# Kernel tuning notes

Hardware: AMD Instinct MI355X
Metric: run time of the kernel (lower is better)

Reference implementation:

```python
import jax, jax.numpy as jnp
import numpy as np

B, N, DIM, H, DH, PD = 2, 1024, 768, 8, 64, 4
EPS = 1e-8


def setup_inputs() -> dict:
    key = jax.random.key(0)
    ks = jax.random.split(key, 12)
    w = lambda k, shp: jax.random.normal(k, shp, dtype=jnp.float32) * 0.02
    return {
        "x": jax.random.normal(ks[0], (B, N, DIM), dtype=jnp.float32),
        "rotations": jax.random.normal(ks[1], (B, N, 3, 3), dtype=jnp.float32),
        "translations": jax.random.normal(ks[2], (B, N, 3), dtype=jnp.float32),
        "W_sq": w(ks[3], (H * DH, DIM)),
        "W_sk": w(ks[4], (H * DH, DIM)),
        "W_sv": w(ks[5], (H * DH, DIM)),
        "W_pq": w(ks[6], (H * PD * 3, DIM)),
        "W_pk": w(ks[7], (H * PD * 3, DIM)),
        "W_pv": w(ks[8], (H * PD * 3, DIM)),
        "point_weights": jax.random.normal(ks[9], (H,), dtype=jnp.float32),
        "W_out": w(ks[10], (DIM, H * (DH + PD * 4))),
        "b_out": jax.random.normal(ks[11], (DIM,), dtype=jnp.float32) * 0.02,
    }


def reference(x, rotations, translations, W_sq, W_sk, W_sv, W_pq, W_pk, W_pv, point_weights, W_out, b_out):
    b, n, _ = x.shape
    h, dh, pd = H, DH, PD
    scalar_scale = (2 * dh) ** -0.5           # num_attn_logits=2
    point_scale = (2 * pd * (9 / 2)) ** -0.5

    # scalar q/k/v: [b,h,n,dh]
    qs = (x @ W_sq.T).reshape(b, n, h, dh).transpose(0, 2, 1, 3)
    ks = (x @ W_sk.T).reshape(b, n, h, dh).transpose(0, 2, 1, 3)
    vs = (x @ W_sv.T).reshape(b, n, h, dh).transpose(0, 2, 1, 3)

    # point q/k/v: [b,h,n,pd,3]
    qp = (x @ W_pq.T).reshape(b, n, h, pd, 3).transpose(0, 2, 1, 3, 4)
    kp = (x @ W_pk.T).reshape(b, n, h, pd, 3).transpose(0, 2, 1, 3, 4)
    vp = (x @ W_pv.T).reshape(b, n, h, pd, 3).transpose(0, 2, 1, 3, 4)

    t = translations[:, None, :, None, :]  # [b,1,n,1,3]
    # global-frame points: p_c = sum_r R[n,c,r] * p[d,r] + t
    qp = jnp.einsum('bncr,bhndr->bhndc', rotations, qp) + t
    kp = jnp.einsum('bncr,bhndr->bhndc', rotations, kp) + t
    vp = jnp.einsum('bncr,bhndr->bhndc', rotations, vp) + t

    # scalar attention logits [b,h,i,j]
    logits = jnp.einsum('bhid,bhjd->bhij', qs, ks) * scalar_scale

    # point distance term: sum_{d,c} (q-k)^2 = |q|^2 + |k|^2 - 2 q.k (no [i,j,d,c] tensor)
    q2 = jnp.sum(qp ** 2, axis=(-1, -2))  # [b,h,i]
    k2 = jnp.sum(kp ** 2, axis=(-1, -2))  # [b,h,j]
    qk = jnp.einsum('bhidc,bhjdc->bhij', qp, kp)
    point_dist = q2[..., :, None] + k2[..., None, :] - 2.0 * qk

    pw = jax.nn.softplus(point_weights)[None, :, None, None]  # [1,h,1,1]
    logits = logits - 0.5 * (point_dist * pw * point_scale)

    attn = jax.nn.softmax(logits, axis=-1)

    rs = jnp.einsum('bhij,bhjd->bhid', attn, vs)          # [b,h,n,dh]
    rp = jnp.einsum('bhij,bhjdc->bhidc', attn, vp)        # [b,h,n,pd,3]
    # back to local frame: R^T (p - t)
    rp = jnp.einsum('bnrc,bhndr->bhndc', rotations, rp - t)
    rn = jnp.sqrt(jnp.sum(rp ** 2, axis=-1) + EPS)        # [b,h,n,pd]

    rs = rs.transpose(0, 2, 1, 3).reshape(b, n, h * dh)
    rp_f = rp.transpose(0, 2, 1, 3, 4).reshape(b, n, h * pd * 3)
    rn = rn.transpose(0, 2, 1, 3).reshape(b, n, h * pd)

    results = jnp.concatenate([rs, rp_f, rn], axis=-1)    # [b,n,640]
    return results @ W_out.T + b_out
```

## Files before the change

### kernel.cpp

```cpp
#include <hip/hip_runtime.h>
#include <hip/hip_bf16.h>
#include <math.h>

#define B_  2
#define N_  1024
#define DIM_ 768
#define H_  8
#define DH_ 64
#define PD_ 4
#define NPROJ 1824
#define NPAD  1920
#define BH_ (B_*H_)
#define FDIM 640

#define OFF_RS   0u
#define OFF_RP   (OFF_RS + (size_t)BH_*N_*DH_)
#define OFF_PRAW (OFF_RP + (size_t)BH_*N_*12)
#define OFF_QA   (OFF_PRAW + (size_t)B_*N_*288)
#define OFF_KA   (OFF_QA + (size_t)BH_*N_*96/2)
#define OFF_VT   (OFF_KA + (size_t)BH_*N_*96/2)
#define OFF_XB   (OFF_VT + (size_t)BH_*80*N_/2)
#define OFF_WB   (OFF_XB + (size_t)B_*N_*DIM_/2)
#define OFF_FB   OFF_XB
#define OFF_WOB  OFF_WB

typedef __attribute__((ext_vector_type(8))) short bf16x8;
typedef __attribute__((ext_vector_type(4))) float f32x4;

__device__ __forceinline__ float dot4(float4 a, float4 b) {
    return a.x*b.x + a.y*b.y + a.z*b.z + a.w*b.w;
}
__device__ __forceinline__ unsigned short f2bf(float f) {
    __hip_bfloat16 h = __float2bfloat16(f);
    return *reinterpret_cast<unsigned short*>(&h);
}

__global__ __launch_bounds__(256) void k_cvt_x(
    const float* __restrict__ x, unsigned short* __restrict__ xb)
{
    int i = blockIdx.x * 256 + threadIdx.x;
    if (i >= (B_*N_*DIM_)/4) return;
    float4 v = reinterpret_cast<const float4*>(x)[i];
    ushort4 o;
    o.x = f2bf(v.x); o.y = f2bf(v.y); o.z = f2bf(v.z); o.w = f2bf(v.w);
    reinterpret_cast<ushort4*>(xb)[i] = o;
}

__global__ __launch_bounds__(256) void k_cvt_w(
    const float* __restrict__ Wsq, const float* __restrict__ Wsk,
    const float* __restrict__ Wsv, const float* __restrict__ Wpq,
    const float* __restrict__ Wpk, const float* __restrict__ Wpv,
    unsigned short* __restrict__ wb)
{
    int i = blockIdx.x * 256 + threadIdx.x;
    if (i >= (NPAD*DIM_)/4) return;
    int row = i / (DIM_/4);
    int c4  = i % (DIM_/4);
    ushort4 o;
    if (row >= NPROJ) {
        o.x = o.y = o.z = o.w = 0;
    } else {
        const float* W;
        if      (row < 512)  W = Wsq + (size_t)row*DIM_;
        else if (row < 1024) W = Wsk + (size_t)(row-512)*DIM_;
        else if (row < 1536) W = Wsv + (size_t)(row-1024)*DIM_;
        else if (row < 1632) W = Wpq + (size_t)(row-1536)*DIM_;
        else if (row < 1728) W = Wpk + (size_t)(row-1632)*DIM_;
        else                 W = Wpv + (size_t)(row-1728)*DIM_;
        float4 v = reinterpret_cast<const float4*>(W)[c4];
        o.x = f2bf(v.x); o.y = f2bf(v.y); o.z = f2bf(v.z); o.w = f2bf(v.w);
    }
    reinterpret_cast<ushort4*>(wb)[i] = o;
}

__global__ __launch_bounds__(256) void k_cvt_wout(
    const float* __restrict__ Wout, unsigned short* __restrict__ wob)
{
    int i = blockIdx.x * 256 + threadIdx.x;
    if (i >= (DIM_*FDIM)/4) return;
    float4 v = reinterpret_cast<const float4*>(Wout)[i];
    ushort4 o;
    o.x = f2bf(v.x); o.y = f2bf(v.y); o.z = f2bf(v.z); o.w = f2bf(v.w);
    reinterpret_cast<ushort4*>(wob)[i] = o;
}

__global__ __launch_bounds__(256) void k_proj_mfma(
    const unsigned short* __restrict__ xb,
    const unsigned short* __restrict__ wb,
    float* __restrict__ ws)
{
    __shared__ unsigned short sAB[2*128*32];
    const int tid  = threadIdx.x;
    const int lane = tid & 63;
    const int wid  = tid >> 6;
    const int mt = blockIdx.x & 15;
    const int nt = blockIdx.x >> 4;
    const int row0 = mt*128;
    const int col0 = nt*128;
    const int wr = (wid >> 1)*64;
    const int wc = (wid & 1)*64;

    f32x4 acc[4][4];
    #pragma unroll
    for (int m = 0; m < 4; ++m)
        #pragma unroll
        for (int n = 0; n < 4; ++n) acc[m][n] = (f32x4){0.f,0.f,0.f,0.f};

    for (int kt = 0; kt < DIM_/32; ++kt) {
        __syncthreads();
        #pragma unroll
        for (int t = 0; t < 4; ++t) {
            int chunk = t*4 + wid;
            int tile  = chunk >> 3;
            int crow  = (chunk & 7) * 16;
            int grow  = (tile ? col0 : row0) + crow + (lane >> 2);
            const unsigned short* gsrc = (tile ? wb : xb)
                + (size_t)grow*DIM_ + kt*32 + (lane & 3)*8;
            __builtin_amdgcn_global_load_lds(
                (const __attribute__((address_space(1))) void*)gsrc,
                (__attribute__((address_space(3))) void*)(sAB + chunk*512),
                16, 0, 0);
        }
        __syncthreads();

        bf16x8 a[4], b[4];
        #pragma unroll
        for (int m = 0; m < 4; ++m)
            a[m] = *reinterpret_cast<const bf16x8*>(
                sAB + ((wr + m*16 + (lane & 15))*32 + (lane >> 4)*8));
        #pragma unroll
        for (int n = 0; n < 4; ++n)
            b[n] = *reinterpret_cast<const bf16x8*>(
                sAB + 128*32 + ((wc + n*16 + (lane & 15))*32 + (lane >> 4)*8));
        #pragma unroll
        for (int m = 0; m < 4; ++m)
            #pragma unroll
            for (int n = 0; n < 4; ++n)
                acc[m][n] = __builtin_amdgcn_mfma_f32_16x16x32_bf16(
                    a[m], b[n], acc[m][n], 0, 0, 0);
    }

    unsigned short* qa = (unsigned short*)(ws + OFF_QA);
    unsigned short* ka = (unsigned short*)(ws + OFF_KA);
    unsigned short* vt = (unsigned short*)(ws + OFF_VT);
    float* praw = ws + OFF_PRAW;
    const float ss = 0.08838834764831845f;

    #pragma unroll
    for (int n = 0; n < 4; ++n) {
        int o = col0 + wc + n*16 + (lane & 15);
        if (o >= NPROJ) continue;
        #pragma unroll
        for (int m = 0; m < 4; ++m) {
            #pragma unroll
            for (int j = 0; j < 4; ++j) {
                int r = row0 + wr + m*16 + (lane >> 4)*4 + j;
                int bb = r >> 10, nn = r & (N_-1);
                float v = acc[m][n][j];
                if (o < 512) {
                    int h = o >> 6, c = o & 63;
                    qa[((size_t)(bb*H_ + h)*N_ + nn)*96 + c] = f2bf(v*ss);
                } else if (o < 1024) {
                    int oo = o - 512; int h = oo >> 6, c = oo & 63;
                    ka[((size_t)(bb*H_ + h)*N_ + nn)*96 + c] = f2bf(v);
                } else if (o < 1536) {
                    int oo = o - 1024; int h = oo >> 6, c = oo & 63;
                    vt[((size_t)(bb*H_ + h)*80 + c)*N_ + nn] = f2bf(v);
                } else {
                    praw[(size_t)r*288 + (o - 1536)] = v;
                }
            }
        }
    }
}

__global__ __launch_bounds__(128) void k_prep(
    const float* __restrict__ rot_g,
    const float* __restrict__ trans_g,
    const float* __restrict__ pw_g,
    float* __restrict__ ws)
{
    __shared__ float R[9], T[3];
    __shared__ float rot[3][8][4][3];
    __shared__ float p2[2][8][4];
    __shared__ float q2t[8], k2t[8], coefs[8];
    const int tid = threadIdx.x;
    const int row = blockIdx.x;
    const int b = row >> 10, n = row & (N_-1);

    if (tid < 9)  R[tid] = rot_g[(size_t)row*9 + tid];
    if (tid >= 9 && tid < 12) T[tid-9] = trans_g[(size_t)row*3 + (tid-9)];
    if (tid >= 16 && tid < 24) {
        float pw = pw_g[tid-16];
        coefs[tid-16] = 0.5f * log1pf(__expf(pw)) * (1.0f/6.0f);
    }
    __syncthreads();
    if (tid < 96) {
        int which = tid >> 5, idx = tid & 31;
        int h = idx >> 2, pd = idx & 3;
        const float* p = ws + OFF_PRAW + (size_t)row*288 + which*96 + h*12 + pd*3;
        float px = p[0], py = p[1], pz = p[2];
        float c0 = R[0]*px + R[1]*py + R[2]*pz + T[0];
        float c1 = R[3]*px + R[4]*py + R[5]*pz + T[1];
        float c2 = R[6]*px + R[7]*py + R[8]*pz + T[2];
        rot[which][h][pd][0] = c0;
        rot[which][h][pd][1] = c1;
        rot[which][h][pd][2] = c2;
        if (which < 2) p2[which][h][pd] = c0*c0 + c1*c1 + c2*c2;
    }
    __syncthreads();
    if (tid < 16) {
        int w = tid >> 3, h = tid & 7;
        float s = p2[w][h][0] + p2[w][h][1] + p2[w][h][2] + p2[w][h][3];
        if (w) k2t[h] = s; else q2t[h] = s;
    }
    __syncthreads();

    unsigned short* qa = (unsigned short*)(ws + OFF_QA);
    unsigned short* ka = (unsigned short*)(ws + OFF_KA);
    unsigned short* vt = (unsigned short*)(ws + OFF_VT);

    for (int i = tid; i < 256; i += 128) {
        int h = i >> 5, c = i & 31;
        float qv, kv;
        if (c < 12)      { qv = rot[0][h][c/3][c%3] * 2.f * coefs[h]; kv = rot[1][h][c/3][c%3]; }
        else if (c == 12){ qv = q2t[h];  kv = -coefs[h]; }
        else if (c == 13){ qv = 1.f;     kv = -coefs[h]*k2t[h]; }
        else             { qv = 0.f;     kv = 0.f; }
        size_t base = ((size_t)(b*H_ + h)*N_ + n)*96 + 64 + c;
        qa[base] = f2bf(qv);
        ka[base] = f2bf(kv);
    }
    {
        int h = tid >> 4, r = tid & 15;
        float vv = (r < 12) ? rot[2][h][r/3][r%3] : 0.f;
        vt[((size_t)(b*H_ + h)*80 + 64 + r)*N_ + n] = f2bf(vv);
    }
}

#define VPAD 72
#define APAD 84
__global__ __launch_bounds__(512, 4) void k_attn_mfma(
    const unsigned short* __restrict__ qa_g,
    const unsigned short* __restrict__ ka_g,
    const unsigned short* __restrict__ vt_g,
    float* __restrict__ ws)
{
    __shared__ unsigned short sP[8][16*VPAD];
    __shared__ float sAcc[3][2][16][APAD];
    __shared__ float sML[3][2][16][2];

    const int tid  = threadIdx.x;
    const int lane = tid & 63;
    const int wid  = tid >> 6;
    const int lo = lane & 15;
    const int hi = lane >> 4;
    const int bid = blockIdx.x;
    const int Lb = (bid & 7)*64 + (bid >> 3);
    const int bh = Lb >> 5;
    const int qt = Lb & 31;
    const int q0 = qt * 32;
    const int qh = wid & 1;
    const int kq = wid >> 1;
    const int mrow = qh * 16;

    const unsigned short* Qa = qa_g + (size_t)bh*N_*96;
    const unsigned short* Ka = ka_g + (size_t)bh*N_*96;
    const unsigned short* Vt = vt_g + (size_t)bh*80*N_;

    bf16x8 qfr[3];
    {
        int qrow = q0 + mrow + lo;
        #pragma unroll
        for (int c = 0; c < 3; ++c)
            qfr[c] = *reinterpret_cast<const bf16x8*>(
                Qa + (size_t)qrow*96 + c*32 + hi*8);
    }

    f32x4 acc[5];
    #pragma unroll
    for (int d = 0; d < 5; ++d) acc[d] = (f32x4){0.f,0.f,0.f,0.f};
    float m[4] = {-1e30f,-1e30f,-1e30f,-1e30f};
    float l[4] = {0.f,0.f,0.f,0.f};

    for (int it = 0; it < 4; ++it) {
        const int j0 = (kq*4 + it)*64;

        bf16x8 kb[3][4];
        #pragma unroll
        for (int c = 0; c < 3; ++c)
            #pragma unroll
            for (int t = 0; t < 4; ++t)
                kb[c][t] = *reinterpret_cast<const bf16x8*>(
                    Ka + (size_t)(j0 + t*16 + lo)*96 + c*32 + hi*8);

        f32x4 s[4];
        #pragma unroll
        for (int t = 0; t < 4; ++t) s[t] = (f32x4){0.f,0.f,0.f,0.f};
        #pragma unroll
        for (int c = 0; c < 3; ++c)
            #pragma unroll
            for (int t = 0; t < 4; ++t)
                s[t] = __builtin_amdgcn_mfma_f32_16x16x32_bf16(qfr[c], kb[c][t], s[t], 0, 0, 0);

        bf16x8 vb[2][5];
        #pragma unroll
        for (int kk = 0; kk < 2; ++kk)
            #pragma unroll
            for (int dt = 0; dt < 5; ++dt)
                vb[kk][dt] = *reinterpret_cast<const bf16x8*>(
                    Vt + (size_t)(dt*16 + lo)*N_ + j0 + kk*32 + hi*8);

        float scl[4];
        #pragma unroll
        for (int r = 0; r < 4; ++r) {
            float v = fmaxf(fmaxf(s[0][r], s[1][r]), fmaxf(s[2][r], s[3][r]));
            v = fmaxf(v, __shfl_xor(v, 1));
            v = fmaxf(v, __shfl_xor(v, 2));
            v = fmaxf(v, __shfl_xor(v, 4));
            v = fmaxf(v, __shfl_xor(v, 8));
            float mn = fmaxf(m[r], v);
            scl[r] = __expf(m[r] - mn);
            m[r] = mn;
        }
        float ps[4] = {0.f,0.f,0.f,0.f};
        #pragma unroll
        for (int t = 0; t < 4; ++t) {
            #pragma unroll
            for (int r = 0; r < 4; ++r) {
                float p = __expf(s[t][r] - m[r]);
                ps[r] += p;
                sP[wid][(hi*4 + r)*VPAD + t*16 + lo] = f2bf(p);
            }
        }
        #pragma unroll
        for (int r = 0; r < 4; ++r) {
            float v = ps[r];
            v += __shfl_xor(v, 1);
            v += __shfl_xor(v, 2);
            v += __shfl_xor(v, 4);
            v += __shfl_xor(v, 8);
            l[r] = l[r]*scl[r] + v;
        }
        #pragma unroll
        for (int d = 0; d < 5; ++d)
            #pragma unroll
            for (int r = 0; r < 4; ++r) acc[d][r] *= scl[r];

        #pragma unroll
        for (int kk = 0; kk < 2; ++kk) {
            bf16x8 pa = *reinterpret_cast<const bf16x8*>(
                &sP[wid][lo*VPAD + kk*32 + hi*8]);
            #pragma unroll
            for (int dt = 0; dt < 5; ++dt)
                acc[dt] = __builtin_amdgcn_mfma_f32_16x16x32_bf16(pa, vb[kk][dt], acc[dt], 0, 0, 0);
        }
    }

    if (kq > 0) {
        #pragma unroll
        for (int r = 0; r < 4; ++r) {
            int rl = hi*4 + r;
            #pragma unroll
            for (int dt = 0; dt < 5; ++dt)
                sAcc[kq-1][qh][rl][dt*16 + lo] = acc[dt][r];
            if (lo == 0) { sML[kq-1][qh][rl][0] = m[r]; sML[kq-1][qh][rl][1] = l[r]; }
        }
    }
    __syncthreads();
    if (kq == 0) {
        float* ws_rs = ws + OFF_RS + (size_t)bh*N_*DH_;
        float* ws_rp = ws + OFF_RP + (size_t)bh*N_*12;
        #pragma unroll
        for (int r = 0; r < 4; ++r) {
            int rl = hi*4 + r;
            float mp[3], lp[3];
            float mm = m[r];
            #pragma unroll
            for (int p = 0; p < 3; ++p) {
                mp[p] = sML[p][qh][rl][0];
                lp[p] = sML[p][qh][rl][1];
                mm = fmaxf(mm, mp[p]);
            }
            float f0 = __expf(m[r] - mm);
            float Lsum = l[r]*f0;
            float fp[3];
            #pragma unroll
            for (int p = 0; p < 3; ++p) {
                fp[p] = __expf(mp[p] - mm);
                Lsum += lp[p]*fp[p];
            }
            float inv = 1.f / Lsum;
            int i = q0 + mrow + rl;
            #pragma unroll
            for (int dt = 0; dt < 5; ++dt) {
                float val = acc[dt][r]*f0;
                #pragma unroll
                for (int p = 0; p < 3; ++p)
                    val += sAcc[p][qh][rl][dt*16 + lo]*fp[p];
                val *= inv;
                int d = dt*16 + lo;
                if (d < 64)
                    ws_rs[(size_t)i*DH_ + d] = val;
                else if (d - 64 < 12)
                    ws_rp[(size_t)i*12 + (d - 64)] = val;
            }
        }
    }
}

__global__ __launch_bounds__(256) void k_fin_prep(
    const float* __restrict__ rotations,
    const float* __restrict__ translations,
    const float* __restrict__ ws,
    unsigned short* __restrict__ fb)
{
    __shared__ float sF[8][FDIM];
    const int tid = threadIdx.x;
    const int row0 = blockIdx.x * 8;
    const int b = row0 >> 10;
    const float* ws_rs = ws + OFF_RS;
    const float* ws_rp = ws + OFF_RP;

    for (int i = tid; i < 8*512; i += 256) {
        int r = i >> 9, f = i & 511;
        int h = f >> 6, c = f & 63;
        int n = (row0 & (N_-1)) + r;
        sF[r][f] = ws_rs[(((size_t)(b*H_ + h))*N_ + n)*DH_ + c];
    }
    {
        int r = tid >> 5;
        int idx = tid & 31;
        int h = idx >> 2, pd = idx & 3;
        int row = row0 + r;
        int n = row & (N_-1);
        const float* rp = ws_rp + (((size_t)(b*H_ + h))*N_ + n)*12 + pd*3;
        const float* R = rotations + (size_t)row*9;
        const float* T = translations + (size_t)row*3;
        float d0 = rp[0] - T[0], d1 = rp[1] - T[1], d2 = rp[2] - T[2];
        float l0 = R[0]*d0 + R[3]*d1 + R[6]*d2;
        float l1 = R[1]*d0 + R[4]*d1 + R[7]*d2;
        float l2 = R[2]*d0 + R[5]*d1 + R[8]*d2;
        sF[r][512 + h*12 + pd*3 + 0] = l0;
        sF[r][512 + h*12 + pd*3 + 1] = l1;
        sF[r][512 + h*12 + pd*3 + 2] = l2;
        sF[r][608 + h*4 + pd] = sqrtf(l0*l0 + l1*l1 + l2*l2 + 1e-8f);
    }
    __syncthreads();

    #pragma unroll
    for (int r = 0; r < 8; ++r) {
        for (int f = tid; f < FDIM; f += 256) {
            fb[(size_t)(row0 + r)*FDIM + f] = f2bf(sF[r][f]);
        }
    }
}

__global__ __launch_bounds__(256) void k_out_mfma(
    const unsigned short* __restrict__ fb,
    const unsigned short* __restrict__ wob,
    const float* __restrict__ bout,
    float* __restrict__ out)
{
    __shared__ unsigned short sAB[2*128*32];
    const int tid  = threadIdx.x;
    const int lane = tid & 63;
    const int wid  = tid >> 6;
    const int mt = blockIdx.x & 15;
    const int nt = blockIdx.x >> 4;
    const int row0 = mt*128;
    const int col0 = nt*128;
    const int wr = (wid >> 1)*64;
    const int wc = (wid & 1)*64;

    f32x4 acc[4][4];
    #pragma unroll
    for (int m = 0; m < 4; ++m)
        #pragma unroll
        for (int n = 0; n < 4; ++n) acc[m][n] = (f32x4){0.f,0.f,0.f,0.f};

    for (int kt = 0; kt < FDIM/32; ++kt) {
        __syncthreads();
        #pragma unroll
        for (int t = 0; t < 4; ++t) {
            int chunk = t*4 + wid;
            int tile  = chunk >> 3;
            int crow  = (chunk & 7) * 16;
            int grow  = (tile ? col0 : row0) + crow + (lane >> 2);
            const unsigned short* gsrc = (tile ? wob : fb)
                + (size_t)grow*FDIM + kt*32 + (lane & 3)*8;
            __builtin_amdgcn_global_load_lds(
                (const __attribute__((address_space(1))) void*)gsrc,
                (__attribute__((address_space(3))) void*)(sAB + chunk*512),
                16, 0, 0);
        }
        __syncthreads();

        bf16x8 a[4], b[4];
        #pragma unroll
        for (int m = 0; m < 4; ++m)
            a[m] = *reinterpret_cast<const bf16x8*>(
                sAB + ((wr + m*16 + (lane & 15))*32 + (lane >> 4)*8));
        #pragma unroll
        for (int n = 0; n < 4; ++n)
            b[n] = *reinterpret_cast<const bf16x8*>(
                sAB + 128*32 + ((wc + n*16 + (lane & 15))*32 + (lane >> 4)*8));
        #pragma unroll
        for (int m = 0; m < 4; ++m)
            #pragma unroll
            for (int n = 0; n < 4; ++n)
                acc[m][n] = __builtin_amdgcn_mfma_f32_16x16x32_bf16(
                    a[m], b[n], acc[m][n], 0, 0, 0);
    }

    #pragma unroll
    for (int n = 0; n < 4; ++n) {
        int o = col0 + wc + n*16 + (lane & 15);
        float bo = bout[o];
        #pragma unroll
        for (int m = 0; m < 4; ++m) {
            #pragma unroll
            for (int j = 0; j < 4; ++j) {
                int r = row0 + wr + m*16 + (lane >> 4)*4 + j;
                out[(size_t)r*DIM_ + o] = acc[m][n][j] + bo;
            }
        }
    }
}

extern "C" void kernel_launch(void* const* d_in, const int* in_sizes, int n_in,
                              void* d_out, int out_size, void* d_ws, size_t ws_size,
                              hipStream_t stream) {
    const float* x            = (const float*)d_in[0];
    const float* rotations    = (const float*)d_in[1];
    const float* translations = (const float*)d_in[2];
    const float* Wsq          = (const float*)d_in[3];
    const float* Wsk          = (const float*)d_in[4];
    const float* Wsv          = (const float*)d_in[5];
    const float* Wpq          = (const float*)d_in[6];
    const float* Wpk          = (const float*)d_in[7];
    const float* Wpv          = (const float*)d_in[8];
    const float* pweights     = (const float*)d_in[9];
    const float* Wout         = (const float*)d_in[10];
    const float* bout         = (const float*)d_in[11];
    float* out = (float*)d_out;
    float* ws  = (float*)d_ws;

    unsigned short* xb  = (unsigned short*)(ws + OFF_XB);
    unsigned short* wb  = (unsigned short*)(ws + OFF_WB);
    unsigned short* qa  = (unsigned short*)(ws + OFF_QA);
    unsigned short* ka  = (unsigned short*)(ws + OFF_KA);
    unsigned short* vt  = (unsigned short*)(ws + OFF_VT);
    unsigned short* fb  = (unsigned short*)(ws + OFF_FB);
    unsigned short* wob = (unsigned short*)(ws + OFF_WOB);

    k_cvt_x<<<(B_*N_*DIM_/4 + 255)/256, 256, 0, stream>>>(x, xb);
    k_cvt_w<<<(NPAD*DIM_/4 + 255)/256, 256, 0, stream>>>(Wsq, Wsk, Wsv, Wpq, Wpk, Wpv, wb);
    k_proj_mfma<<<16*15, 256, 0, stream>>>(xb, wb, ws);
    k_prep<<<B_*N_, 128, 0, stream>>>(rotations, translations, pweights, ws);
    k_attn_mfma<<<BH_*32, 512, 0, stream>>>(qa, ka, vt, ws);
    k_cvt_wout<<<(DIM_*FDIM/4 + 255)/256, 256, 0, stream>>>(Wout, wob);
    k_fin_prep<<<B_*N_/8, 256, 0, stream>>>(rotations, translations, ws, fb);
    k_out_mfma<<<16*6, 256, 0, stream>>>(fb, wob, bout, out);
}
```

Measured before the change: 100.9 us.

## Replace LDS-staged GEMMs with single-wave direct-register MFMA tiles and XCD-aware mapping

Both the projection GEMM and the output GEMM drop the shared-memory staged 128x128 tiles with four waves. Each block is now a single wave computing a 64x64 tile, loading fragments directly from global memory into registers with a two-stage double buffer. Block indices are remapped so consecutive tiles land on the same XCD. This removes LDS traffic and barriers and raises the block count to fill more CUs. The cost is no operand sharing between waves, so global and L2 traffic per FLOP goes up.

```diff
diff --git a/kernel.cpp b/kernel.cpp
--- a/kernel.cpp
+++ b/kernel.cpp
@@ -27,9 +27,6 @@
 typedef __attribute__((ext_vector_type(8))) short bf16x8;
 typedef __attribute__((ext_vector_type(4))) float f32x4;
 
-__device__ __forceinline__ float dot4(float4 a, float4 b) {
-    return a.x*b.x + a.y*b.y + a.z*b.z + a.w*b.w;
-}
 __device__ __forceinline__ unsigned short f2bf(float f) {
     __hip_bfloat16 h = __float2bfloat16(f);
     return *reinterpret_cast<unsigned short*>(&h);
@@ -84,21 +81,47 @@
     reinterpret_cast<ushort4*>(wob)[i] = o;
 }
 
-__global__ __launch_bounds__(256) void k_proj_mfma(
+__device__ __forceinline__ void load_frags(
+    const unsigned short* __restrict__ A0,
+    const unsigned short* __restrict__ B0,
+    int koff, int ld, bf16x8 a[4], bf16x8 b[4])
+{
+    #pragma unroll
+    for (int m = 0; m < 4; ++m)
+        a[m] = *reinterpret_cast<const bf16x8*>(A0 + (size_t)m*16*ld + koff);
+    #pragma unroll
+    for (int n = 0; n < 4; ++n)
+        b[n] = *reinterpret_cast<const bf16x8*>(B0 + (size_t)n*16*ld + koff);
+}
+
+__device__ __forceinline__ void mfma16(
+    const bf16x8 a[4], const bf16x8 b[4], f32x4 acc[4][4])
+{
+    #pragma unroll
+    for (int m = 0; m < 4; ++m)
+        #pragma unroll
+        for (int n = 0; n < 4; ++n)
+            acc[m][n] = __builtin_amdgcn_mfma_f32_16x16x32_bf16(
+                a[m], b[n], acc[m][n], 0, 0, 0);
+}
+
+__global__ __launch_bounds__(64, 1) void k_proj_mfma(
     const unsigned short* __restrict__ xb,
     const unsigned short* __restrict__ wb,
     float* __restrict__ ws)
 {
-    __shared__ unsigned short sAB[2*128*32];
-    const int tid  = threadIdx.x;
-    const int lane = tid & 63;
-    const int wid  = tid >> 6;
-    const int mt = blockIdx.x & 15;
-    const int nt = blockIdx.x >> 4;
-    const int row0 = mt*128;
-    const int col0 = nt*128;
-    const int wr = (wid >> 1)*64;
-    const int wc = (wid & 1)*64;
+    const int lane = threadIdx.x;
+    const int lo = lane & 15;
+    const int hi = lane >> 4;
+    const int bid = blockIdx.x;
+    const int L = (bid & 7)*120 + (bid >> 3);
+    const int mt = L / 30;
+    const int nt = L % 30;
+    const int row0 = mt*64;
+    const int col0 = nt*64;
+
+    const unsigned short* A0 = xb + (size_t)(row0 + lo)*DIM_ + hi*8;
+    const unsigned short* B0 = wb + (size_t)(col0 + lo)*DIM_ + hi*8;
 
     f32x4 acc[4][4];
     #pragma unroll
@@ -106,38 +129,14 @@
         #pragma unroll
         for (int n = 0; n < 4; ++n) acc[m][n] = (f32x4){0.f,0.f,0.f,0.f};
 
-    for (int kt = 0; kt < DIM_/32; ++kt) {
-        __syncthreads();
-        #pragma unroll
-        for (int t = 0; t < 4; ++t) {
-            int chunk = t*4 + wid;
-            int tile  = chunk >> 3;
-            int crow  = (chunk & 7) * 16;
-            int grow  = (tile ? col0 : row0) + crow + (lane >> 2);
-            const unsigned short* gsrc = (tile ? wb : xb)
-                + (size_t)grow*DIM_ + kt*32 + (lane & 3)*8;
-            __builtin_amdgcn_global_load_lds(
-                (const __attribute__((address_space(1))) void*)gsrc,
-                (__attribute__((address_space(3))) void*)(sAB + chunk*512),
-                16, 0, 0);
-        }
-        __syncthreads();
-
-        bf16x8 a[4], b[4];
-        #pragma unroll
-        for (int m = 0; m < 4; ++m)
-            a[m] = *reinterpret_cast<const bf16x8*>(
-                sAB + ((wr + m*16 + (lane & 15))*32 + (lane >> 4)*8));
-        #pragma unroll
-        for (int n = 0; n < 4; ++n)
-            b[n] = *reinterpret_cast<const bf16x8*>(
-                sAB + 128*32 + ((wc + n*16 + (lane & 15))*32 + (lane >> 4)*8));
-        #pragma unroll
-        for (int m = 0; m < 4; ++m)
-            #pragma unroll
-            for (int n = 0; n < 4; ++n)
-                acc[m][n] = __builtin_amdgcn_mfma_f32_16x16x32_bf16(
-                    a[m], b[n], acc[m][n], 0, 0, 0);
+    bf16x8 aA[4], bA[4], aB[4], bB[4];
+    load_frags(A0, B0, 0, DIM_, aA, bA);
+    for (int kt = 0; kt < DIM_/32; kt += 2) {
+        load_frags(A0, B0, (kt+1)*32, DIM_, aB, bB);
+        mfma16(aA, bA, acc);
+        if (kt + 2 < DIM_/32)
+            load_frags(A0, B0, (kt+2)*32, DIM_, aA, bA);
+        mfma16(aB, bB, acc);
     }
 
     unsigned short* qa = (unsigned short*)(ws + OFF_QA);
@@ -148,13 +147,13 @@
 
     #pragma unroll
     for (int n = 0; n < 4; ++n) {
-        int o = col0 + wc + n*16 + (lane & 15);
+        int o = col0 + n*16 + lo;
         if (o >= NPROJ) continue;
         #pragma unroll
         for (int m = 0; m < 4; ++m) {
             #pragma unroll
             for (int j = 0; j < 4; ++j) {
-                int r = row0 + wr + m*16 + (lane >> 4)*4 + j;
+                int r = row0 + m*16 + hi*4 + j;
                 int bb = r >> 10, nn = r & (N_-1);
                 float v = acc[m][n][j];
                 if (o < 512) {
@@ -456,22 +455,24 @@
     }
 }
 
-__global__ __launch_bounds__(256) void k_out_mfma(
+__global__ __launch_bounds__(64, 1) void k_out_mfma(
     const unsigned short* __restrict__ fb,
     const unsigned short* __restrict__ wob,
     const float* __restrict__ bout,
     float* __restrict__ out)
 {
-    __shared__ unsigned short sAB[2*128*32];
-    const int tid  = threadIdx.x;
-    const int lane = tid & 63;
-    const int wid  = tid >> 6;
-    const int mt = blockIdx.x & 15;
-    const int nt = blockIdx.x >> 4;
-    const int row0 = mt*128;
-    const int col0 = nt*128;
-    const int wr = (wid >> 1)*64;
-    const int wc = (wid & 1)*64;
+    const int lane = threadIdx.x;
+    const int lo = lane & 15;
+    const int hi = lane >> 4;
+    const int bid = blockIdx.x;
+    const int L = (bid & 7)*48 + (bid >> 3);
+    const int mt = L / 12;
+    const int nt = L % 12;
+    const int row0 = mt*64;
+    const int col0 = nt*64;
+
+    const unsigned short* A0 = fb  + (size_t)(row0 + lo)*FDIM + hi*8;
+    const unsigned short* B0 = wob + (size_t)(col0 + lo)*FDIM + hi*8;
 
     f32x4 acc[4][4];
     #pragma unroll
@@ -479,49 +480,25 @@
         #pragma unroll
         for (int n = 0; n < 4; ++n) acc[m][n] = (f32x4){0.f,0.f,0.f,0.f};
 
-    for (int kt = 0; kt < FDIM/32; ++kt) {
-        __syncthreads();
-        #pragma unroll
-        for (int t = 0; t < 4; ++t) {
-            int chunk = t*4 + wid;
-            int tile  = chunk >> 3;
-            int crow  = (chunk & 7) * 16;
-            int grow  = (tile ? col0 : row0) + crow + (lane >> 2);
-            const unsigned short* gsrc = (tile ? wob : fb)
-                + (size_t)grow*FDIM + kt*32 + (lane & 3)*8;
-            __builtin_amdgcn_global_load_lds(
-                (const __attribute__((address_space(1))) void*)gsrc,
-                (__attribute__((address_space(3))) void*)(sAB + chunk*512),
-                16, 0, 0);
-        }
-        __syncthreads();
-
-        bf16x8 a[4], b[4];
-        #pragma unroll
-        for (int m = 0; m < 4; ++m)
-            a[m] = *reinterpret_cast<const bf16x8*>(
-                sAB + ((wr + m*16 + (lane & 15))*32 + (lane >> 4)*8));
-        #pragma unroll
-        for (int n = 0; n < 4; ++n)
-            b[n] = *reinterpret_cast<const bf16x8*>(
-                sAB + 128*32 + ((wc + n*16 + (lane & 15))*32 + (lane >> 4)*8));
-        #pragma unroll
-        for (int m = 0; m < 4; ++m)
-            #pragma unroll
-            for (int n = 0; n < 4; ++n)
-                acc[m][n] = __builtin_amdgcn_mfma_f32_16x16x32_bf16(
-                    a[m], b[n], acc[m][n], 0, 0, 0);
+    bf16x8 aA[4], bA[4], aB[4], bB[4];
+    load_frags(A0, B0, 0, FDIM, aA, bA);
+    for (int kt = 0; kt < FDIM/32; kt += 2) {
+        load_frags(A0, B0, (kt+1)*32, FDIM, aB, bB);
+        mfma16(aA, bA, acc);
+        if (kt + 2 < FDIM/32)
+            load_frags(A0, B0, (kt+2)*32, FDIM, aA, bA);
+        mfma16(aB, bB, acc);
     }
 
     #pragma unroll
     for (int n = 0; n < 4; ++n) {
-        int o = col0 + wc + n*16 + (lane & 15);
+        int o = col0 + n*16 + lo;
         float bo = bout[o];
         #pragma unroll
         for (int m = 0; m < 4; ++m) {
             #pragma unroll
             for (int j = 0; j < 4; ++j) {
-                int r = row0 + wr + m*16 + (lane >> 4)*4 + j;
+                int r = row0 + m*16 + hi*4 + j;
                 out[(size_t)r*DIM_ + o] = acc[m][n][j] + bo;
             }
         }
@@ -556,10 +533,10 @@
 
     k_cvt_x<<<(B_*N_*DIM_/4 + 255)/256, 256, 0, stream>>>(x, xb);
     k_cvt_w<<<(NPAD*DIM_/4 + 255)/256, 256, 0, stream>>>(Wsq, Wsk, Wsv, Wpq, Wpk, Wpv, wb);
-    k_proj_mfma<<<16*15, 256, 0, stream>>>(xb, wb, ws);
+    k_proj_mfma<<<960, 64, 0, stream>>>(xb, wb, ws);
     k_prep<<<B_*N_, 128, 0, stream>>>(rotations, translations, pweights, ws);
     k_attn_mfma<<<BH_*32, 512, 0, stream>>>(qa, ka, vt, ws);
     k_cvt_wout<<<(DIM_*FDIM/4 + 255)/256, 256, 0, stream>>>(Wout, wob);
     k_fin_prep<<<B_*N_/8, 256, 0, stream>>>(rotations, translations, ws, fb);
-    k_out_mfma<<<16*6, 256, 0, stream>>>(fb, wob, bout, out);
-}
+    k_out_mfma<<<384, 64, 0, stream>>>(fb, wob, bout, out);
+}
```

New measurement: 109.0 us. 1.08x slower.
